# Optimization experiments

Measured on AMD Instinct MI355X. Metric: run time of the kernel, lower is better.

The kernel has to match this reference:

```python
import jax, jax.numpy as jnp
import numpy as np


def setup_inputs() -> dict:
    key = jax.random.key(0)
    ks = jax.random.split(key, 8)
    B, C, W, H = 4, 256, 64, 64
    Cq = C // 8
    return {
        "input": jax.random.normal(ks[0], (B, C, W, H), dtype=jnp.float32),
        "Wf": jax.random.normal(ks[1], (Cq, C), dtype=jnp.float32) * 0.05,
        "bf": jax.random.normal(ks[2], (Cq,), dtype=jnp.float32) * 0.05,
        "Wg": jax.random.normal(ks[3], (Cq, C), dtype=jnp.float32) * 0.05,
        "bg": jax.random.normal(ks[4], (Cq,), dtype=jnp.float32) * 0.05,
        "Wh": jax.random.normal(ks[5], (C, C), dtype=jnp.float32) * 0.05,
        "bh": jax.random.normal(ks[6], (C,), dtype=jnp.float32) * 0.05,
        "gamma": jax.random.normal(ks[7], (1,), dtype=jnp.float32),
    }


def reference(input, Wf, bf, Wg, bg, Wh, bh, gamma):
    # input: [B, C, W, H]; SAGAN self-attention over N = W*H spatial tokens.
    B, C, W, H = input.shape
    N = W * H
    x = input.reshape(B, C, N)
    # 1x1 Conv1d == per-token linear projection over channels.
    f = jnp.einsum('oc,bcn->bon', Wf, x) + bf[None, :, None]  # [B, C/8, N]
    g = jnp.einsum('oc,bcn->bon', Wg, x) + bg[None, :, None]  # [B, C/8, N]
    h = jnp.einsum('oc,bcn->bon', Wh, x) + bh[None, :, None]  # [B, C,   N]
    # s = f^T g -> [B, N, N]; softmax over last dim (columns / g-tokens).
    s = jnp.einsum('bon,bom->bnm', f, g)
    attention = jax.nn.softmax(s, axis=-1)
    # out = h @ attention^T : out[b,c,m] = sum_n h[b,c,n] * attention[b,m,n]
    out = jnp.einsum('bcn,bmn->bcm', h, attention)
    out = out.reshape(B, C, W, H)
    return gamma[0] * out + input
```

## Files before the change

### kernel.cpp

```cpp
#include <hip/hip_runtime.h>

typedef _Float16 half8 __attribute__((ext_vector_type(8)));
typedef _Float16 half4 __attribute__((ext_vector_type(4)));
typedef unsigned int uintx2 __attribute__((ext_vector_type(2)));
typedef unsigned int uintx4 __attribute__((ext_vector_type(4)));
typedef float floatx16 __attribute__((ext_vector_type(16)));

#define MFMA_F16(A, B, C) __builtin_amdgcn_mfma_f32_32x32x16_f16(A, B, C, 0, 0, 0)

constexpr int Bn = 4;
constexpr int Cc = 256;
constexpr int Cq = 32;
constexpr int Nn = 4096;
constexpr float LOG2E = 1.44269504088896340736f;


__device__ inline floatx16 zero16() {
  floatx16 z;
#pragma unroll
  for (int i = 0; i < 16; ++i) z[i] = 0.f;
  return z;
}

__device__ inline unsigned int pkrtz(float a, float b) {
  return __builtin_bit_cast(unsigned int, __builtin_amdgcn_cvt_pkrtz(a, b));
}

__global__ __launch_bounds__(256) void k_wconv(
    const float* __restrict__ Wf, const float* __restrict__ Wg,
    const float* __restrict__ Wh, _Float16* __restrict__ Wfh,
    _Float16* __restrict__ Wgh, _Float16* __restrict__ Whh) {
  int e = (blockIdx.x * 256 + threadIdx.x) * 4;
  const float* src;
  _Float16* dst;
  float sc = 1.f;
  if (e < 8192) { src = Wf + e; dst = Wfh + e; sc = LOG2E; }
  else if (e < 16384) { src = Wg + (e - 8192); dst = Wgh + (e - 8192); }
  else { src = Wh + (e - 16384); dst = Whh + (e - 16384); }
  float4 v = *(const float4*)src;
  half4 o;
  o[0] = (_Float16)(v.x * sc); o[1] = (_Float16)(v.y * sc);
  o[2] = (_Float16)(v.z * sc); o[3] = (_Float16)(v.w * sc);
  *(half4*)dst = o;
}

__global__ __launch_bounds__(512) void k_proj(
    const float* __restrict__ x,
    const _Float16* __restrict__ Wfh, const float* __restrict__ bf,
    const _Float16* __restrict__ Wgh, const float* __restrict__ bg,
    const _Float16* __restrict__ Whh, const float* __restrict__ bh,
    _Float16* __restrict__ Q, _Float16* __restrict__ K4,
    _Float16* __restrict__ V8) {
  __shared__ float xs[32][260];
  __shared__ _Float16 vtr[8][1280];
  int tid = threadIdx.x;
  int w = tid >> 6, lane = tid & 63;
  int ml = lane & 31, h = lane >> 5;
  int b = blockIdx.x >> 7, nt = blockIdx.x & 127;
  int n0 = nt * 32;

  {
    int c = tid >> 3;
    int nl = (tid & 7) * 4;
    const float* xp = x + (size_t)b * Cc * Nn + n0 + nl;
#pragma unroll
    for (int pass = 0; pass < 4; ++pass) {
      int cc = c + pass * 64;
      float4 v = *(const float4*)(xp + (size_t)cc * Nn);
      xs[nl + 0][cc] = v.x;
      xs[nl + 1][cc] = v.y;
      xs[nl + 2][cc] = v.z;
      xs[nl + 3][cc] = v.w;
    }
  }
  __syncthreads();

  half8 bfr[16];
#pragma unroll
  for (int kc = 0; kc < 16; ++kc) {
    const float* xp = &xs[ml][kc * 16 + h * 8];
    half8 f;
#pragma unroll
    for (int j = 0; j < 8; ++j) f[j] = (_Float16)xp[j];
    bfr[kc] = f;
  }

  for (int t = w; t < 10; t += 8) {
    const _Float16* W;
    const float* bias;
    float bscale = 1.f;
    int o0 = 0;
    if (t == 0) { W = Wfh; bias = bf; bscale = LOG2E; }
    else if (t == 1) { W = Wgh; bias = bg; }
    else { W = Whh + (size_t)(t - 2) * 32 * Cc; bias = bh + (t - 2) * 32; o0 = (t - 2) * 32; }

    floatx16 acc = zero16();
    const _Float16* wp = W + (size_t)ml * Cc + h * 8;
#pragma unroll
    for (int kc = 0; kc < 16; ++kc) {
      half8 a = *(const half8*)(wp + kc * 16);
      acc = MFMA_F16(a, bfr[kc], acc);
    }

    if (t == 0) {
      _Float16* op = Q + ((size_t)b * Nn + n0 + ml) * Cq;
#pragma unroll
      for (int qd = 0; qd < 4; ++qd) {
        float4 bq = *(const float4*)(bias + 8 * qd + 4 * h);
        const float* bqp = (const float*)&bq;
#pragma unroll
        for (int i = 0; i < 4; ++i) {
          int crow = i + 8 * qd + 4 * h;
          op[crow] = (_Float16)(acc[4 * qd + i] + bqp[i] * bscale);
        }
      }
    } else if (t == 1) {
#pragma unroll
      for (int qd = 0; qd < 4; ++qd) {
        float4 bq = *(const float4*)(bias + 8 * qd + 4 * h);
        const float* bqp = (const float*)&bq;
#pragma unroll
        for (int i = 0; i < 4; ++i) {
          int crow = i + 8 * qd + 4 * h;
          K4[(((size_t)b * 4 + (crow >> 3)) * Nn + n0 + ml) * 8 + (crow & 7)] =
              (_Float16)(acc[4 * qd + i] + bqp[i]);
        }
      }
    } else {
      _Float16* vs = vtr[w];
#pragma unroll
      for (int qd = 0; qd < 4; ++qd) {
        float4 bq = *(const float4*)(bias + 8 * qd + 4 * h);
        const float* bqp = (const float*)&bq;
#pragma unroll
        for (int i = 0; i < 4; ++i) {
          int crow = i + 8 * qd + 4 * h;
          vs[crow * 40 + ml] = (_Float16)(acc[4 * qd + i] + bqp[i]);
        }
      }
      const _Float16* rs = vtr[w] + ml * 40;
#pragma unroll
      for (int r = 0; r < 2; ++r) {
        int tg = h * 2 + r;
        half8 vv = *(const half8*)(rs + tg * 8);
        *(half8*)(V8 + (((size_t)b * 512 + (n0 >> 3) + tg) * 256 + o0 + ml) * 8) = vv;
      }
    }
  }
}

__global__ __launch_bounds__(512) void k_rowmax(const _Float16* __restrict__ Q,
                                                const _Float16* __restrict__ K4,
                                                float* __restrict__ M) {
  __shared__ float red[8][32];
  int tid = threadIdx.x, w = tid >> 6, lane = tid & 63;
  int ml = lane & 31, h = lane >> 5;
  int b = blockIdx.x >> 7, mt = blockIdx.x & 127;
  int m0 = mt * 32;
  const _Float16* qp = Q + ((size_t)b * Nn + m0 + ml) * Cq + h * 8;
  half8 qb0 = *(const half8*)(qp);
  half8 qb1 = *(const half8*)(qp + 16);
  const _Float16* kp0 = K4 + (((size_t)b * 4 + h) * Nn + w * 512 + ml) * 8;
  const _Float16* kp1 = K4 + (((size_t)b * 4 + 2 + h) * Nn + w * 512 + ml) * 8;
  float mx = -3.0e38f;
  for (int t = 0; t < 16; ++t) {
    floatx16 s = zero16();
    half8 k0 = *(const half8*)(kp0 + (size_t)t * 32 * 8);
    half8 k1 = *(const half8*)(kp1 + (size_t)t * 32 * 8);
    s = MFMA_F16(k0, qb0, s);
    s = MFMA_F16(k1, qb1, s);
#pragma unroll
    for (int i = 0; i < 16; ++i) mx = fmaxf(mx, s[i]);
  }
  mx = fmaxf(mx, __shfl_xor(mx, 32, 64));
  if (h == 0) red[w][ml] = mx;
  __syncthreads();
  if (tid < 32) {
    float m2 = red[0][tid];
#pragma unroll
    for (int i = 1; i < 8; ++i) m2 = fmaxf(m2, red[i][tid]);
    M[(size_t)b * Nn + m0 + tid] = m2;
  }
}

__device__ inline void otree_write(float2* dst, const floatx16* o) {
#pragma unroll
  for (int cb = 0; cb < 8; ++cb)
#pragma unroll
    for (int rp = 0; rp < 8; ++rp)
      dst[(cb * 8 + rp) * 64] = make_float2(o[cb][2 * rp], o[cb][2 * rp + 1]);
}

__device__ inline void otree_add(const float2* src, floatx16* o) {
#pragma unroll
  for (int cb = 0; cb < 8; ++cb)
#pragma unroll
    for (int rp = 0; rp < 8; ++rp) {
      float2 v = src[(cb * 8 + rp) * 64];
      o[cb][2 * rp] += v.x;
      o[cb][2 * rp + 1] += v.y;
    }
}

__global__ __launch_bounds__(512, 2) void k_attn(
    const _Float16* __restrict__ Q, const _Float16* __restrict__ K4,
    const _Float16* __restrict__ V8, const float* __restrict__ M,
    const float* __restrict__ xin, const float* __restrict__ gamma,
    float* __restrict__ out) {
  __shared__ float Ored[4 * 8192];
  __shared__ float lred[8][32];
  int tid = threadIdx.x, w = tid >> 6, lane = tid & 63;
  int ml = lane & 31, h = lane >> 5;
  int mh = w >> 2, nw = w & 3;
  int bx = blockIdx.x;
  int mt = bx & 63, b = bx >> 6;
  int mb = mt * 64;
  int m0 = mb + mh * 32;

  const _Float16* qp = Q + ((size_t)b * Nn + m0 + ml) * Cq + h * 8;
  half8 qb0 = *(const half8*)(qp);
  half8 qb1 = *(const half8*)(qp + 16);
  float Mv = M[(size_t)b * Nn + m0 + ml];
  float g = gamma[0];
  float lacc = 0.f;

  const _Float16* k4b0 = K4 + (((size_t)b * 4 + h) * Nn + nw * 32 + ml) * 8;
  const _Float16* k4b1 = K4 + (((size_t)b * 4 + 2 + h) * Nn + nw * 32 + ml) * 8;
  const _Float16* v8b = V8 + (((size_t)b * 512 + nw * 4 + h) * 256 + ml) * 8;

  floatx16 o[8];
#pragma unroll
  for (int i = 0; i < 8; ++i) o[i] = zero16();

  half8 k0 = *(const half8*)(k4b0);
  half8 k1 = *(const half8*)(k4b1);

  for (int it = 0; it < 32; ++it) {
    floatx16 s = zero16();
    s = MFMA_F16(k0, qb0, s);
    s = MFMA_F16(k1, qb1, s);
    k0 = *(const half8*)(k4b0 + (size_t)(it + 1) * 1024);
    k1 = *(const half8*)(k4b1 + (size_t)(it + 1) * 1024);
    float p[16];
#pragma unroll
    for (int i = 0; i < 16; ++i) p[i] = __builtin_amdgcn_exp2f(s[i] - Mv);
#pragma unroll
    for (int i = 0; i < 16; ++i) lacc += p[i];
    unsigned int c0 = pkrtz(p[0], p[1]),  c1 = pkrtz(p[2], p[3]);
    unsigned int c2 = pkrtz(p[4], p[5]),  c3 = pkrtz(p[6], p[7]);
    unsigned int c4 = pkrtz(p[8], p[9]),  c5 = pkrtz(p[10], p[11]);
    unsigned int c6 = pkrtz(p[12], p[13]), c7 = pkrtz(p[14], p[15]);
    uintx2 t02 = __builtin_amdgcn_permlane32_swap(c0, c2, false, false);
    uintx2 t13 = __builtin_amdgcn_permlane32_swap(c1, c3, false, false);
    uintx2 t46 = __builtin_amdgcn_permlane32_swap(c4, c6, false, false);
    uintx2 t57 = __builtin_amdgcn_permlane32_swap(c5, c7, false, false);
    uintx4 f0v = {t02.x, t13.x, t02.y, t13.y};
    uintx4 f1v = {t46.x, t57.x, t46.y, t57.y};
    half8 pf0 = __builtin_bit_cast(half8, f0v);
    half8 pf1 = __builtin_bit_cast(half8, f1v);
    const _Float16* vp = v8b + (size_t)it * 32768;
#pragma unroll
    for (int cb = 0; cb < 8; ++cb) {
      half8 vf0 = *(const half8*)(vp + cb * 256);
      o[cb] = MFMA_F16(vf0, pf0, o[cb]);
    }
#pragma unroll
    for (int cb = 0; cb < 8; ++cb) {
      half8 vf1 = *(const half8*)(vp + 4096 + cb * 256);
      o[cb] = MFMA_F16(vf1, pf1, o[cb]);
    }
  }

  lacc += __shfl_xor(lacc, 32, 64);
  if (h == 0) lred[w][ml] = lacc;

  float2* Ored2 = (float2*)Ored;
  int lofs = h * 32 + ml;
  float2* rg0 = Ored2 + (size_t)(mh * 2) * 4096 + lofs;
  float2* rg1 = Ored2 + (size_t)(mh * 2 + 1) * 4096 + lofs;
  if (nw == 2) otree_write(rg0, o);
  if (nw == 3) otree_write(rg1, o);
  __syncthreads();
  if (nw == 0) otree_add(rg0, o);
  if (nw == 1) otree_add(rg1, o);
  __syncthreads();
  if (nw == 1) otree_write(rg1, o);
  __syncthreads();
  if (nw == 0) { otree_add(rg1, o); otree_write(rg0, o); }
  __syncthreads();

  float lv0 = lred[0][ml] + lred[1][ml] + lred[2][ml] + lred[3][ml];
  float lv1 = lred[4][ml] + lred[5][ml] + lred[6][ml] + lred[7][ml];
  float sc0 = g / lv0;
  float sc1 = g / lv1;
  const float2* src0 = Ored2 + lofs;
  const float2* src1 = Ored2 + (size_t)2 * 4096 + lofs;
  size_t obase0 = ((size_t)b * 256 + w * 32) * (size_t)Nn + mb + ml;
  size_t obase1 = obase0 + 32;
#pragma unroll
  for (int rp = 0; rp < 8; ++rp) {
    int r = 2 * rp;
    int cA = (r & 3) + 8 * (r >> 2) + 4 * h;
    size_t oa0 = obase0 + (size_t)cA * Nn;
    size_t oa1 = obase1 + (size_t)cA * Nn;
    float2 v0 = src0[(w * 8 + rp) * 64];
    float2 v1 = src1[(w * 8 + rp) * 64];
    out[oa0] = sc0 * v0.x + xin[oa0];
    out[oa0 + Nn] = sc0 * v0.y + xin[oa0 + Nn];
    out[oa1] = sc1 * v1.x + xin[oa1];
    out[oa1 + Nn] = sc1 * v1.y + xin[oa1 + Nn];
  }
}

extern "C" void kernel_launch(void* const* d_in, const int* in_sizes, int n_in,
                              void* d_out, int out_size, void* d_ws,
                              size_t ws_size, hipStream_t stream) {
  const float* x = (const float*)d_in[0];
  const float* Wf = (const float*)d_in[1];
  const float* bf = (const float*)d_in[2];
  const float* Wg = (const float*)d_in[3];
  const float* bg = (const float*)d_in[4];
  const float* Wh = (const float*)d_in[5];
  const float* bh = (const float*)d_in[6];
  const float* gamma = (const float*)d_in[7];
  float* out = (float*)d_out;

  char* ws = (char*)d_ws;
  _Float16* Q  = (_Float16*)(ws);
  _Float16* K4 = (_Float16*)(ws + 1048576);
  _Float16* V8 = (_Float16*)(ws + 2097152);
  float*    M  = (float*)   (ws + 10485760);
  _Float16* Wfh = (_Float16*)(ws + 10551296);
  _Float16* Wgh = (_Float16*)(ws + 10567680);
  _Float16* Whh = (_Float16*)(ws + 10584064);

  k_wconv<<<dim3(80), dim3(256), 0, stream>>>(Wf, Wg, Wh, Wfh, Wgh, Whh);
  k_proj<<<dim3(512), dim3(512), 0, stream>>>(x, Wfh, bf, Wgh, bg, Whh, bh, Q, K4, V8);
  k_rowmax<<<dim3(512), dim3(512), 0, stream>>>(Q, K4, M);
  k_attn<<<dim3(256), dim3(512), 0, stream>>>(Q, K4, V8, M, x, gamma, out);
}
```

Baseline: 157.0 us.

## Apply value projection after attention instead of before

```diff
diff --git a/kernel.cpp b/kernel.cpp
--- a/kernel.cpp
+++ b/kernel.cpp
@@ -44,15 +44,13 @@
   *(half4*)dst = o;
 }
 
-__global__ __launch_bounds__(512) void k_proj(
+__global__ __launch_bounds__(512) void k_qkv(
     const float* __restrict__ x,
     const _Float16* __restrict__ Wfh, const float* __restrict__ bf,
     const _Float16* __restrict__ Wgh, const float* __restrict__ bg,
-    const _Float16* __restrict__ Whh, const float* __restrict__ bh,
     _Float16* __restrict__ Q, _Float16* __restrict__ K4,
     _Float16* __restrict__ V8) {
   __shared__ float xs[32][260];
-  __shared__ _Float16 vtr[8][1280];
   int tid = threadIdx.x;
   int w = tid >> 6, lane = tid & 63;
   int ml = lane & 31, h = lane >> 5;
@@ -75,24 +73,20 @@
   }
   __syncthreads();
 
-  half8 bfr[16];
-#pragma unroll
-  for (int kc = 0; kc < 16; ++kc) {
-    const float* xp = &xs[ml][kc * 16 + h * 8];
-    half8 f;
-#pragma unroll
-    for (int j = 0; j < 8; ++j) f[j] = (_Float16)xp[j];
-    bfr[kc] = f;
-  }
-
-  for (int t = w; t < 10; t += 8) {
-    const _Float16* W;
-    const float* bias;
-    float bscale = 1.f;
-    int o0 = 0;
-    if (t == 0) { W = Wfh; bias = bf; bscale = LOG2E; }
-    else if (t == 1) { W = Wgh; bias = bg; }
-    else { W = Whh + (size_t)(t - 2) * 32 * Cc; bias = bh + (t - 2) * 32; o0 = (t - 2) * 32; }
+  if (w < 2) {
+    half8 bfr[16];
+#pragma unroll
+    for (int kc = 0; kc < 16; ++kc) {
+      const float* xp = &xs[ml][kc * 16 + h * 8];
+      half8 f;
+#pragma unroll
+      for (int j = 0; j < 8; ++j) f[j] = (_Float16)xp[j];
+      bfr[kc] = f;
+    }
+
+    const _Float16* W = (w == 0) ? Wfh : Wgh;
+    const float* bias = (w == 0) ? bf : bg;
+    float bscale = (w == 0) ? LOG2E : 1.f;
 
     floatx16 acc = zero16();
     const _Float16* wp = W + (size_t)ml * Cc + h * 8;
@@ -102,7 +96,7 @@
       acc = MFMA_F16(a, bfr[kc], acc);
     }
 
-    if (t == 0) {
+    if (w == 0) {
       _Float16* op = Q + ((size_t)b * Nn + n0 + ml) * Cq;
 #pragma unroll
       for (int qd = 0; qd < 4; ++qd) {
@@ -114,7 +108,7 @@
           op[crow] = (_Float16)(acc[4 * qd + i] + bqp[i] * bscale);
         }
       }
-    } else if (t == 1) {
+    } else {
 #pragma unroll
       for (int qd = 0; qd < 4; ++qd) {
         float4 bq = *(const float4*)(bias + 8 * qd + 4 * h);
@@ -126,26 +120,17 @@
               (_Float16)(acc[4 * qd + i] + bqp[i]);
         }
       }
-    } else {
-      _Float16* vs = vtr[w];
-#pragma unroll
-      for (int qd = 0; qd < 4; ++qd) {
-        float4 bq = *(const float4*)(bias + 8 * qd + 4 * h);
-        const float* bqp = (const float*)&bq;
-#pragma unroll
-        for (int i = 0; i < 4; ++i) {
-          int crow = i + 8 * qd + 4 * h;
-          vs[crow * 40 + ml] = (_Float16)(acc[4 * qd + i] + bqp[i]);
-        }
-      }
-      const _Float16* rs = vtr[w] + ml * 40;
-#pragma unroll
-      for (int r = 0; r < 2; ++r) {
-        int tg = h * 2 + r;
-        half8 vv = *(const half8*)(rs + tg * 8);
-        *(half8*)(V8 + (((size_t)b * 512 + (n0 >> 3) + tg) * 256 + o0 + ml) * 8) = vv;
-      }
-    }
+    }
+  }
+
+#pragma unroll
+  for (int gi = 0; gi < 2; ++gi) {
+    int gidx = tid + gi * 512;
+    int nbl = gidx >> 8, c = gidx & 255;
+    half8 vv;
+#pragma unroll
+    for (int i = 0; i < 8; ++i) vv[i] = (_Float16)xs[nbl * 8 + i][c];
+    *(half8*)(V8 + (((size_t)b * 512 + (n0 >> 3) + nbl) * 256 + c) * 8) = vv;
   }
 }
 
@@ -205,6 +190,7 @@
 __global__ __launch_bounds__(512, 2) void k_attn(
     const _Float16* __restrict__ Q, const _Float16* __restrict__ K4,
     const _Float16* __restrict__ V8, const float* __restrict__ M,
+    const _Float16* __restrict__ Whh, const float* __restrict__ bh,
     const float* __restrict__ xin, const float* __restrict__ gamma,
     float* __restrict__ out) {
   __shared__ float Ored[4 * 8192];
@@ -291,24 +277,47 @@
 
   float lv0 = lred[0][ml] + lred[1][ml] + lred[2][ml] + lred[3][ml];
   float lv1 = lred[4][ml] + lred[5][ml] + lred[6][ml] + lred[7][ml];
-  float sc0 = g / lv0;
-  float sc1 = g / lv1;
-  const float2* src0 = Ored2 + lofs;
-  const float2* src1 = Ored2 + (size_t)2 * 4096 + lofs;
-  size_t obase0 = ((size_t)b * 256 + w * 32) * (size_t)Nn + mb + ml;
-  size_t obase1 = obase0 + 32;
-#pragma unroll
-  for (int rp = 0; rp < 8; ++rp) {
-    int r = 2 * rp;
-    int cA = (r & 3) + 8 * (r >> 2) + 4 * h;
-    size_t oa0 = obase0 + (size_t)cA * Nn;
-    size_t oa1 = obase1 + (size_t)cA * Nn;
-    float2 v0 = src0[(w * 8 + rp) * 64];
-    float2 v1 = src1[(w * 8 + rp) * 64];
-    out[oa0] = sc0 * v0.x + xin[oa0];
-    out[oa0 + Nn] = sc0 * v0.y + xin[oa0 + Nn];
-    out[oa1] = sc1 * v1.x + xin[oa1];
-    out[oa1 + Nn] = sc1 * v1.y + xin[oa1 + Nn];
+  float il0 = g / lv0;
+  float il1 = g / lv1;
+  int offs[8];
+#pragma unroll
+  for (int j = 0; j < 8; ++j) {
+    int u = h * 8 + j;
+    int rb = (u & 3) | ((u >> 3) << 2);
+    int hw = (u >> 2) & 1;
+    offs[j] = (rb >> 1) * 128 + hw * 64 + 2 * ml + (rb & 1);
+  }
+  const float* R0 = Ored;
+  const float* R1 = Ored + 2 * 8192;
+  int c0 = w * 32;
+  const _Float16* whp = Whh + (size_t)(c0 + ml) * 256 + h * 8;
+  floatx16 d0 = zero16(), d1 = zero16();
+#pragma unroll
+  for (int kq = 0; kq < 16; ++kq) {
+    half8 a = *(const half8*)(whp + kq * 16);
+    float q0[8], q1[8];
+#pragma unroll
+    for (int j = 0; j < 8; ++j) {
+      q0[j] = R0[kq * 512 + offs[j]] * il0;
+      q1[j] = R1[kq * 512 + offs[j]] * il1;
+    }
+    uintx4 b0v = {pkrtz(q0[0], q0[1]), pkrtz(q0[2], q0[3]),
+                  pkrtz(q0[4], q0[5]), pkrtz(q0[6], q0[7])};
+    uintx4 b1v = {pkrtz(q1[0], q1[1]), pkrtz(q1[2], q1[3]),
+                  pkrtz(q1[4], q1[5]), pkrtz(q1[6], q1[7])};
+    d0 = MFMA_F16(a, __builtin_bit_cast(half8, b0v), d0);
+    d1 = MFMA_F16(a, __builtin_bit_cast(half8, b1v), d1);
+  }
+
+  size_t ob = (size_t)b * 256 * (size_t)Nn;
+#pragma unroll
+  for (int r = 0; r < 16; ++r) {
+    int c = c0 + (r & 3) + 8 * (r >> 2) + 4 * h;
+    float bias = g * bh[c];
+    size_t oa0 = ob + (size_t)c * Nn + mb + ml;
+    size_t oa1 = oa0 + 32;
+    out[oa0] = d0[r] + bias + xin[oa0];
+    out[oa1] = d1[r] + bias + xin[oa1];
   }
 }
 
@@ -335,7 +344,7 @@
   _Float16* Whh = (_Float16*)(ws + 10584064);
 
   k_wconv<<<dim3(80), dim3(256), 0, stream>>>(Wf, Wg, Wh, Wfh, Wgh, Whh);
-  k_proj<<<dim3(512), dim3(512), 0, stream>>>(x, Wfh, bf, Wgh, bg, Whh, bh, Q, K4, V8);
+  k_qkv<<<dim3(512), dim3(512), 0, stream>>>(x, Wfh, bf, Wgh, bg, Q, K4, V8);
   k_rowmax<<<dim3(512), dim3(512), 0, stream>>>(Q, K4, M);
-  k_attn<<<dim3(256), dim3(512), 0, stream>>>(Q, K4, V8, M, x, gamma, out);
-}
+  k_attn<<<dim3(256), dim3(512), 0, stream>>>(Q, K4, V8, M, Whh, bh, x, gamma, out);
+}
```

Result: faster. 151.6 us (-3.4%).
